# Performance work log

Measured on AMD Instinct MI355X. Metric: run time of the kernel, lower is better.

The kernel has to match this reference:

```python
import jax, jax.numpy as jnp
import numpy as np

N, E, F_IN, EDIM, H = 50000, 1600000, 128, 16, 4
C1, C2, G, NCLS = 32, 8, 64, 10
NEG_SLOPE = 0.2


def setup_inputs() -> dict:
    key = jax.random.key(0)
    ks = jax.random.split(key, 20)
    s = 0.1
    inp = {
        "x": jax.random.normal(ks[0], (N, F_IN), jnp.float32),
        "edge_index": jax.random.randint(ks[1], (2, E), 0, N, dtype=jnp.int32),
        "edge_attr": jax.random.normal(ks[2], (E, EDIM), jnp.float32),
        "batch": jnp.sort(jax.random.randint(ks[3], (N,), 0, G, dtype=jnp.int32)),
        # layer 1 params (PyG GATConv: shared lin for src/dst, no lin bias)
        "W1": jax.random.normal(ks[4], (F_IN, H * C1), jnp.float32) * s,
        "as1": jax.random.normal(ks[5], (H, C1), jnp.float32) * s,
        "ad1": jax.random.normal(ks[6], (H, C1), jnp.float32) * s,
        "We1": jax.random.normal(ks[7], (EDIM, H * C1), jnp.float32) * s,
        "ae1": jax.random.normal(ks[8], (H, C1), jnp.float32) * s,
        "b1": jnp.zeros((H * C1,), jnp.float32),
        # layer 2 params
        "W2": jax.random.normal(ks[9], (H * C1, H * C2), jnp.float32) * s,
        "as2": jax.random.normal(ks[10], (H, C2), jnp.float32) * s,
        "ad2": jax.random.normal(ks[11], (H, C2), jnp.float32) * s,
        "We2": jax.random.normal(ks[12], (EDIM, H * C2), jnp.float32) * s,
        "ae2": jax.random.normal(ks[13], (H, C2), jnp.float32) * s,
        "b2": jnp.zeros((H * C2,), jnp.float32),
        # final linear
        "Wfc": jax.random.normal(ks[14], (H * C2, NCLS), jnp.float32) * s,
        "bfc": jnp.zeros((NCLS,), jnp.float32),
    }
    return inp


def _add_self_loops(src, dst, edge_attr):
    # PyG default: add_self_loops=True, fill_value='mean' (mean of incoming edge attrs)
    deg = jax.ops.segment_sum(jnp.ones((E,), jnp.float32), dst, num_segments=N)
    loop_attr = jax.ops.segment_sum(edge_attr, dst, num_segments=N) / jnp.maximum(deg, 1.0)[:, None]
    loop = jnp.arange(N, dtype=src.dtype)
    return (jnp.concatenate([src, loop]), jnp.concatenate([dst, loop]),
            jnp.concatenate([edge_attr, loop_attr], axis=0))


def _gat_layer(x, src, dst, ea, W, a_src, a_dst, We, a_e, b, heads, ch):
    n = x.shape[0]
    h = (x @ W).reshape(n, heads, ch)                 # [N,H,C]
    he = (ea @ We).reshape(-1, heads, ch)             # [Ef,H,C]
    al_src = jnp.einsum('nhc,hc->nh', h, a_src)       # [N,H]
    al_dst = jnp.einsum('nhc,hc->nh', h, a_dst)
    al_e = jnp.einsum('ehc,hc->eh', he, a_e)          # [Ef,H]
    alpha = al_src[src] + al_dst[dst] + al_e
    alpha = jax.nn.leaky_relu(alpha, NEG_SLOPE)
    # edge softmax grouped by destination node
    amax = jax.ops.segment_max(alpha, dst, num_segments=n)
    alpha = jnp.exp(alpha - amax[dst])
    denom = jax.ops.segment_sum(alpha, dst, num_segments=n)
    alpha = alpha / (denom[dst] + 1e-16)
    out = jax.ops.segment_sum(h[src] * alpha[..., None], dst, num_segments=n)  # [N,H,C]
    return out.reshape(n, heads * ch) + b


def reference(x, edge_index, edge_attr, batch, W1, as1, ad1, We1, ae1, b1,
              W2, as2, ad2, We2, ae2, b2, Wfc, bfc):
    src, dst = edge_index[0], edge_index[1]
    src, dst, ea = _add_self_loops(src, dst, edge_attr)
    h = jax.nn.relu(_gat_layer(x, src, dst, ea, W1, as1, ad1, We1, ae1, b1, H, C1))
    h = jax.nn.relu(_gat_layer(h, src, dst, ea, W2, as2, ad2, We2, ae2, b2, H, C2))
    # global mean pool over graphs
    cnt = jax.ops.segment_sum(jnp.ones((N,), jnp.float32), batch, num_segments=G)
    pooled = jax.ops.segment_sum(h, batch, num_segments=G) / jnp.maximum(cnt, 1.0)[:, None]
    return pooled @ Wfc + bfc
```

## Files before the change

kernel.cpp:

```cpp
#include <hip/hip_runtime.h>
#include <hip/hip_fp16.h>
#include <math.h>

typedef float4 f4;
#define NEG_SLOPE 0.2f
#define NBMAX 1024
#define BIN_CHUNK 8192

union h4pack { float2 f; __half2 h[2]; };

__global__ void k_prep(const float* __restrict__ We1, const float* __restrict__ ae1,
                       const float* __restrict__ We2, const float* __restrict__ ae2,
                       float* __restrict__ M) {
    int t = threadIdx.x;
    if (t >= 128) return;
    int sel = t >> 6, i = t & 63, d = i >> 2, h = i & 3;
    const float* W  = sel ? We2 : We1;
    const float* ae = sel ? ae2 : ae1;
    int C = sel ? 8 : 32, ncol = sel ? 32 : 128;
    float s = 0.f;
    for (int c = 0; c < C; ++c) s += W[d * ncol + h * C + c] * ae[h * C + c];
    M[sel * 64 + d * 4 + h] = s;
}

__global__ __launch_bounds__(256) void k_bhist(const int* __restrict__ ei,
                                               int* __restrict__ bcnt, int E, int NB) {
    __shared__ int hist[NBMAX];
    for (int i = threadIdx.x; i < NB; i += 256) hist[i] = 0;
    __syncthreads();
    int stride = gridDim.x * 256;
    for (int e = blockIdx.x * 256 + threadIdx.x; e < E; e += stride)
        atomicAdd(&hist[ei[E + e] >> 6], 1);
    __syncthreads();
    for (int i = threadIdx.x; i < NB; i += 256) {
        int h = hist[i];
        if (h) atomicAdd(&bcnt[i], h);
    }
}

__global__ void k_bscan(const int* __restrict__ bcnt, int* __restrict__ bprefix,
                        int* __restrict__ bcursor, int NB) {
    __shared__ int ts[NBMAX];
    int t = threadIdx.x;
    ts[t] = (t < NB) ? bcnt[t] : 0;
    __syncthreads();
    for (int off = 1; off < 1024; off <<= 1) {
        int v = (t >= off) ? ts[t - off] : 0;
        __syncthreads();
        ts[t] += v;
        __syncthreads();
    }
    int excl = (t == 0) ? 0 : ts[t - 1];
    if (t <= NB) {
        bprefix[t] = excl;
        if (t < NB) bcursor[t] = excl;
    }
}

__global__ void k_ale_lin(const float* __restrict__ ea, const float* __restrict__ Mbuf,
                          __half* __restrict__ ale1_e, __half* __restrict__ ale2_e, int E) {
    __shared__ float Ms[128];
    if (threadIdx.x < 128) Ms[threadIdx.x] = Mbuf[threadIdx.x];
    __syncthreads();
    int e = blockIdx.x * 256 + threadIdx.x;
    if (e >= E) return;
    const f4* row = (const f4*)(ea + (size_t)e * 16);
    f4 r0 = row[0], r1 = row[1], r2 = row[2], r3 = row[3];
    float a[16] = { r0.x, r0.y, r0.z, r0.w, r1.x, r1.y, r1.z, r1.w,
                    r2.x, r2.y, r2.z, r2.w, r3.x, r3.y, r3.z, r3.w };
    float s10 = 0.f, s11 = 0.f, s12 = 0.f, s13 = 0.f;
    float s20 = 0.f, s21 = 0.f, s22 = 0.f, s23 = 0.f;
#pragma unroll
    for (int dd = 0; dd < 16; ++dd) {
        float av = a[dd];
        s10 += av * Ms[dd * 4 + 0]; s11 += av * Ms[dd * 4 + 1];
        s12 += av * Ms[dd * 4 + 2]; s13 += av * Ms[dd * 4 + 3];
        s20 += av * Ms[64 + dd * 4 + 0]; s21 += av * Ms[64 + dd * 4 + 1];
        s22 += av * Ms[64 + dd * 4 + 2]; s23 += av * Ms[64 + dd * 4 + 3];
    }
    h4pack p1, p2;
    p1.h[0] = __floats2half2_rn(s10, s11); p1.h[1] = __floats2half2_rn(s12, s13);
    p2.h[0] = __floats2half2_rn(s20, s21); p2.h[1] = __floats2half2_rn(s22, s23);
    ((float2*)ale1_e)[e] = p1.f;
    ((float2*)ale2_e)[e] = p2.f;
}

__global__ __launch_bounds__(256) void k_bin(const int* __restrict__ ei,
                                             int* __restrict__ bcursor,
                                             int2* __restrict__ binned, int E, int NB) {
    __shared__ int hist[NBMAX], base[NBMAX], cur[NBMAX];
    for (int i = threadIdx.x; i < NB; i += 256) { hist[i] = 0; cur[i] = 0; }
    __syncthreads();
    int e0 = blockIdx.x * BIN_CHUNK;
    int e1 = min(e0 + BIN_CHUNK, E);
    for (int e = e0 + threadIdx.x; e < e1; e += 256)
        atomicAdd(&hist[ei[E + e] >> 6], 1);
    __syncthreads();
    for (int i = threadIdx.x; i < NB; i += 256) {
        int h = hist[i];
        if (h) base[i] = atomicAdd(&bcursor[i], h);
    }
    __syncthreads();
    for (int e = e0 + threadIdx.x; e < e1; e += 256) {
        int sr = ei[e], d = ei[E + e];
        int b = d >> 6;
        int loc = base[b] + atomicAdd(&cur[b], 1);
        binned[loc] = make_int2(sr, ((d & 63) << 26) | e);
    }
}

__global__ __launch_bounds__(256) void k_csr(const int2* __restrict__ binned,
                                             const int* __restrict__ bprefix,
                                             int* __restrict__ offsets,
                                             int* __restrict__ csr_src,
                                             int* __restrict__ csr_eid,
                                             int N, int E, int NB) {
    __shared__ int nhist[64], noff[65];
    int b = blockIdx.x;
    if (threadIdx.x < 64) nhist[threadIdx.x] = 0;
    __syncthreads();
    int lo = bprefix[b], hi = bprefix[b + 1];
    for (int s = lo + threadIdx.x; s < hi; s += 256)
        atomicAdd(&nhist[(binned[s].y >> 26) & 63], 1);
    __syncthreads();
    if (threadIdx.x == 0) {
        int run = 0;
        for (int i = 0; i < 64; ++i) { noff[i] = run; run += nhist[i]; }
        noff[64] = run;
    }
    __syncthreads();
    int nlo = b << 6;
    int nbn = min(64, N - nlo);
    if (threadIdx.x < nbn) offsets[nlo + threadIdx.x] = lo + noff[threadIdx.x];
    if (b == NB - 1 && threadIdx.x == 0) offsets[N] = E;
    if (threadIdx.x < 64) nhist[threadIdx.x] = 0;
    __syncthreads();
    for (int s = lo + threadIdx.x; s < hi; s += 256) {
        int2 r = binned[s];
        int dl = (r.y >> 26) & 63;
        int slot = lo + noff[dl] + atomicAdd(&nhist[dl], 1);
        csr_src[slot] = r.x;
        csr_eid[slot] = r.y & 0x03FFFFFF;
    }
}

template<int NOUT, int ROWS>
__global__ __launch_bounds__(256) void k_gemm(const float* __restrict__ X,
                                              const float* __restrict__ W,
                                              __half* __restrict__ Hout, int N) {
    __shared__ __align__(16) float xs[ROWS][128];
    int row0 = blockIdx.x * ROWS;
    int tid = threadIdx.x;
    constexpr int NF4 = ROWS * 32;
    const f4* x4 = (const f4*)X;
    for (int i = tid; i < NF4; i += 256) {
        int r = i >> 5, k4 = i & 31;
        f4 v;
        if (row0 + r < N) v = x4[(size_t)(row0 + r) * 32 + k4];
        else { v.x = v.y = v.z = v.w = 0.f; }
        ((f4*)&xs[r][0])[k4] = v;
    }
    __syncthreads();
    constexpr int GRP = 256 / NOUT;
    constexpr int PR  = ROWS / GRP;
    int col = tid % NOUT, rg = tid / NOUT;
    float acc[PR];
#pragma unroll
    for (int r = 0; r < PR; ++r) acc[r] = 0.f;
    for (int k = 0; k < 128; ++k) {
        float w = W[k * NOUT + col];
#pragma unroll
        for (int r = 0; r < PR; ++r) acc[r] += xs[rg + r * GRP][k] * w;
    }
#pragma unroll
    for (int r = 0; r < PR; ++r) {
        int row = row0 + rg + r * GRP;
        if (row < N) Hout[(size_t)row * NOUT + col] = __float2half(acc[r]);
    }
}

template<int C>
__global__ void k_al(const __half* __restrict__ Hm, const float* __restrict__ as_,
                     const float* __restrict__ ad_, float* __restrict__ als,
                     float* __restrict__ ald, int N) {
    int idx = blockIdx.x * 256 + threadIdx.x;
    int n = idx >> 2, h = idx & 3;
    if (n >= N) return;
    constexpr int CH = C / 4;
    const __half2* h2p = (const __half2*)(Hm + (size_t)n * C + h * CH);
    float a = 0.f, b = 0.f;
#pragma unroll
    for (int c = 0; c < CH / 2; ++c) {
        float2 v = __half22float2(h2p[c]);
        a += v.x * as_[h * CH + 2 * c] + v.y * as_[h * CH + 2 * c + 1];
        b += v.x * ad_[h * CH + 2 * c] + v.y * ad_[h * CH + 2 * c + 1];
    }
    als[n * 4 + h] = a;
    ald[n * 4 + h] = b;
}

__global__ __launch_bounds__(256) void k_alpha_node(const __half* __restrict__ ale_e,
                                                    __half* __restrict__ alpha_csr,
                                                    const int* __restrict__ csr_src,
                                                    const int* __restrict__ csr_eid,
                                                    const float* __restrict__ als,
                                                    const float* __restrict__ ald,
                                                    const int* __restrict__ offsets,
                                                    float* __restrict__ rden,
                                                    float* __restrict__ selfa, int N) {
    int n = (blockIdx.x * 256 + threadIdx.x) >> 6;
    int lane = threadIdx.x & 63;
    if (n >= N) return;
    int j = lane >> 2, h = lane & 3;
    int s0 = offsets[n], s1 = offsets[n + 1];
    float aldn = ald[n * 4 + h];
    float den = 0.f, asum = 0.f;
    for (int base = s0; base < s1; base += 16) {
        int s = base + j;
        if (s < s1) {
            int src = csr_src[s];
            int eid = csr_eid[s];
            float ale = __half2float(ale_e[(size_t)eid * 4 + h]);
            float v = als[src * 4 + h] + aldn + ale;
            v = (v > 0.f) ? v : NEG_SLOPE * v;
            float e = __expf(v);
            alpha_csr[s * 4 + h] = __float2half(e);
            den += e; asum += ale;
        }
    }
    den  += __shfl_xor(den, 4);  den  += __shfl_xor(den, 8);
    den  += __shfl_xor(den, 16); den  += __shfl_xor(den, 32);
    asum += __shfl_xor(asum, 4);  asum += __shfl_xor(asum, 8);
    asum += __shfl_xor(asum, 16); asum += __shfl_xor(asum, 32);
    if (j == 0) {
        float rdeg = 1.f / fmaxf((float)(s1 - s0), 1.f);
        float v = als[n * 4 + h] + aldn + asum * rdeg;
        v = (v > 0.f) ? v : NEG_SLOPE * v;
        float es = __expf(v);
        selfa[n * 4 + h] = es;
        rden[n * 4 + h] = 1.f / (den + es + 1e-16f);
    }
}

__global__ __launch_bounds__(256) void k_aggf128(const __half* __restrict__ h16,
                                                 const __half* __restrict__ alpha16,
                                                 const float* __restrict__ rden,
                                                 const float* __restrict__ selfa,
                                                 const int* __restrict__ offsets,
                                                 const int* __restrict__ csr_src,
                                                 const float* __restrict__ bias,
                                                 float* __restrict__ Out, int N) {
    int n = (blockIdx.x * 256 + threadIdx.x) >> 6;
    int lane = threadIdx.x & 63;
    if (n >= N) return;
    int hd = lane >> 4;
    int s0 = offsets[n], s1 = offsets[n + 1];
    const __half2* H2 = (const __half2*)h16;
    float acc0 = 0.f, acc1 = 0.f;
    int e1 = s1 - 1;
    for (int s = s0; s < s1; s += 8) {
        int srck[8]; float ak[8]; __half2 hvk[8];
#pragma unroll
        for (int k = 0; k < 8; ++k) {
            int sk = min(s + k, e1);
            srck[k] = csr_src[sk];
            ak[k] = (s + k <= e1) ? __half2float(alpha16[(size_t)sk * 4 + hd]) : 0.f;
        }
#pragma unroll
        for (int k = 0; k < 8; ++k) hvk[k] = H2[(size_t)srck[k] * 64 + lane];
#pragma unroll
        for (int k = 0; k < 8; ++k) {
            float2 f = __half22float2(hvk[k]);
            acc0 = fmaf(ak[k], f.x, acc0);
            acc1 = fmaf(ak[k], f.y, acc1);
        }
    }
    float sa = selfa[n * 4 + hd];
    float2 hn = __half22float2(H2[(size_t)n * 64 + lane]);
    acc0 = fmaf(sa, hn.x, acc0);
    acc1 = fmaf(sa, hn.y, acc1);
    float rd = rden[n * 4 + hd];
    float2 bv = ((const float2*)bias)[lane];
    float2 o;
    o.x = fmaxf(fmaf(acc0, rd, bv.x), 0.f);
    o.y = fmaxf(fmaf(acc1, rd, bv.y), 0.f);
    ((float2*)Out)[(size_t)n * 64 + lane] = o;
}

__global__ __launch_bounds__(256) void k_aggf32(const __half* __restrict__ h16,
                                                const __half* __restrict__ alpha16,
                                                const float* __restrict__ rden,
                                                const float* __restrict__ selfa,
                                                const int* __restrict__ offsets,
                                                const int* __restrict__ csr_src,
                                                const float* __restrict__ bias,
                                                float* __restrict__ Out, int N) {
    int n = (blockIdx.x * 256 + threadIdx.x) >> 6;
    int lane = threadIdx.x & 63;
    if (n >= N) return;
    int j = lane >> 4;
    int p = lane & 15;
    int hd = p >> 2;
    int s0 = offsets[n], s1 = offsets[n + 1];
    const __half2* H2 = (const __half2*)h16;
    float acc0 = 0.f, acc1 = 0.f;
    int e1 = s1 - 1;
    for (int s = s0 + j; s < s1; s += 8) {
        int sA = s;
        int sB = min(s + 4, e1);
        int srcA = csr_src[sA], srcB = csr_src[sB];
        float aA = __half2float(alpha16[(size_t)sA * 4 + hd]);
        float aB = (s + 4 <= e1) ? __half2float(alpha16[(size_t)sB * 4 + hd]) : 0.f;
        __half2 hA = H2[(size_t)srcA * 16 + p];
        __half2 hB = H2[(size_t)srcB * 16 + p];
        float2 fA = __half22float2(hA), fB = __half22float2(hB);
        acc0 = fmaf(aA, fA.x, acc0); acc1 = fmaf(aA, fA.y, acc1);
        acc0 = fmaf(aB, fB.x, acc0); acc1 = fmaf(aB, fB.y, acc1);
    }
    acc0 += __shfl_xor(acc0, 16); acc0 += __shfl_xor(acc0, 32);
    acc1 += __shfl_xor(acc1, 16); acc1 += __shfl_xor(acc1, 32);
    if (j == 0) {
        float sa = selfa[n * 4 + hd];
        float2 hn = __half22float2(H2[(size_t)n * 16 + p]);
        acc0 = fmaf(sa, hn.x, acc0);
        acc1 = fmaf(sa, hn.y, acc1);
        float rd = rden[n * 4 + hd];
        float2 bv = ((const float2*)bias)[p];
        float2 o;
        o.x = fmaxf(fmaf(acc0, rd, bv.x), 0.f);
        o.y = fmaxf(fmaf(acc1, rd, bv.y), 0.f);
        ((float2*)Out)[(size_t)n * 16 + p] = o;
    }
}

__global__ void k_gbound(const int* __restrict__ batch, int* __restrict__ gstart, int N, int G) {
    int g = threadIdx.x;
    if (g > G) return;
    int lo = 0, hi = N;
    while (lo < hi) {
        int mid = (lo + hi) >> 1;
        if (batch[mid] < g) lo = mid + 1; else hi = mid;
    }
    gstart[g] = lo;
}

__global__ __launch_bounds__(256) void k_pool_grp(const float* __restrict__ out2,
                                                  const int* __restrict__ gstart,
                                                  float* __restrict__ pooled, int G) {
    __shared__ float red[8][32];
    int g = blockIdx.x;
    int t = threadIdx.x, c = t & 31, r = t >> 5;
    int s0 = gstart[g], s1 = gstart[g + 1];
    float acc = 0.f;
    for (int n = s0 + r; n < s1; n += 8) acc += out2[(size_t)n * 32 + c];
    red[r][c] = acc;
    __syncthreads();
    if (r == 0) {
        float s = red[0][c];
#pragma unroll
        for (int i = 1; i < 8; ++i) s += red[i][c];
        pooled[g * 32 + c] = s;
    }
}

__global__ void k_final(const float* __restrict__ pooled, const int* __restrict__ gstart,
                        const float* __restrict__ Wfc, const float* __restrict__ bfc,
                        float* __restrict__ out) {
    int t = threadIdx.x;
    if (t >= 640) return;
    int g = t / 10, cls = t % 10;
    float rc = 1.f / fmaxf((float)(gstart[g + 1] - gstart[g]), 1.f);
    float acc = bfc[cls];
    for (int c = 0; c < 32; ++c) acc += pooled[g * 32 + c] * rc * Wfc[c * 10 + cls];
    out[g * 10 + cls] = acc;
}

extern "C" void kernel_launch(void* const* d_in, const int* in_sizes, int n_in,
                              void* d_out, int out_size, void* d_ws, size_t ws_size,
                              hipStream_t stream) {
    const float* x    = (const float*)d_in[0];
    const int*   ei   = (const int*)  d_in[1];
    const float* ea   = (const float*)d_in[2];
    const int*   batch= (const int*)  d_in[3];
    const float* W1   = (const float*)d_in[4];
    const float* as1  = (const float*)d_in[5];
    const float* ad1  = (const float*)d_in[6];
    const float* We1  = (const float*)d_in[7];
    const float* ae1  = (const float*)d_in[8];
    const float* b1   = (const float*)d_in[9];
    const float* W2   = (const float*)d_in[10];
    const float* as2  = (const float*)d_in[11];
    const float* ad2  = (const float*)d_in[12];
    const float* We2  = (const float*)d_in[13];
    const float* ae2  = (const float*)d_in[14];
    const float* b2   = (const float*)d_in[15];
    const float* Wfc  = (const float*)d_in[16];
    const float* bfc  = (const float*)d_in[17];
    float* out = (float*)d_out;

    const int N  = in_sizes[3];
    const int E  = in_sizes[1] / 2;
    const int G  = 64;
    const int NB = (N + 63) >> 6;

    char* w = (char*)d_ws;
    size_t off = 0;
    auto alloc = [&](size_t bytes) -> void* {
        void* p = w + off;
        off = (off + bytes + 255) & ~(size_t)255;
        return p;
    };
    int*    bcnt       = (int*)   alloc((size_t)NBMAX * 4);
    int*    bprefix    = (int*)   alloc((size_t)(NBMAX + 1) * 4);
    int*    bcursor    = (int*)   alloc((size_t)NBMAX * 4);
    int*    offsets    = (int*)   alloc((size_t)(N + 1) * 4);
    int2*   binned     = (int2*)  alloc((size_t)E * 8);
    __half* ale1_e     = (__half*)alloc((size_t)E * 4 * 2);
    __half* ale2_e     = (__half*)alloc((size_t)E * 4 * 2);
    int*    csr_src    = (int*)   alloc((size_t)E * 4);
    int*    csr_eid    = (int*)   alloc((size_t)E * 4);
    float*  Mbuf       = (float*) alloc(128 * 4);
    __half* h16        = (__half*)alloc((size_t)N * 128 * 2);
    float*  out1       = (float*) alloc((size_t)N * 128 * 4);
    float*  als        = (float*) alloc((size_t)N * 4 * 4);
    float*  ald        = (float*) alloc((size_t)N * 4 * 4);
    float*  rden       = (float*) alloc((size_t)N * 4 * 4);
    float*  selfa      = (float*) alloc((size_t)N * 4 * 4);
    int*    gstart     = (int*)   alloc((G + 1) * 4);
    float*  pooled     = (float*) alloc(G * 32 * 4);
    __half* alpha_csr  = (__half*)binned;
    float*  out2 = out1;

    const int eb  = (E + 255) / 256;
    const int nb4 = (N + 3) / 4;

    hipMemsetAsync(bcnt, 0, (size_t)NBMAX * 4, stream);

    k_prep<<<1, 128, 0, stream>>>(We1, ae1, We2, ae2, Mbuf);
    k_bhist<<<128, 256, 0, stream>>>(ei, bcnt, E, NB);
    k_bscan<<<1, 1024, 0, stream>>>(bcnt, bprefix, bcursor, NB);
    k_ale_lin<<<eb, 256, 0, stream>>>(ea, Mbuf, ale1_e, ale2_e, E);
    k_bin<<<(E + BIN_CHUNK - 1) / BIN_CHUNK, 256, 0, stream>>>(ei, bcursor, binned, E, NB);
    k_csr<<<NB, 256, 0, stream>>>(binned, bprefix, offsets, csr_src, csr_eid, N, E, NB);
    k_gbound<<<1, 128, 0, stream>>>(batch, gstart, N, G);

    k_gemm<128, 16><<<(N + 15) / 16, 256, 0, stream>>>(x, W1, h16, N);
    k_al<128><<<(N * 4 + 255) / 256, 256, 0, stream>>>(h16, as1, ad1, als, ald, N);
    k_alpha_node<<<nb4, 256, 0, stream>>>(ale1_e, alpha_csr, csr_src, csr_eid, als, ald, offsets, rden, selfa, N);
    k_aggf128<<<nb4, 256, 0, stream>>>(h16, alpha_csr, rden, selfa, offsets, csr_src, b1, out1, N);

    k_gemm<32, 64><<<(N + 63) / 64, 256, 0, stream>>>(out1, W2, h16, N);
    k_al<32><<<(N * 4 + 255) / 256, 256, 0, stream>>>(h16, as2, ad2, als, ald, N);
    k_alpha_node<<<nb4, 256, 0, stream>>>(ale2_e, alpha_csr, csr_src, csr_eid, als, ald, offsets, rden, selfa, N);
    k_aggf32<<<nb4, 256, 0, stream>>>(h16, alpha_csr, rden, selfa, offsets, csr_src, b2, out2, N);

    k_pool_grp<<<G, 256, 0, stream>>>(out2, gstart, pooled, G);
    k_final<<<1, 640, 0, stream>>>(pooled, gstart, Wfc, bfc, out);
}
```

Baseline: 393.1 us.

## Fuse edge-softmax attention computation into the aggregation kernels

Removes the separate per-node alpha kernel and computes unnormalised attention weights, the denominator and the self-loop weight inside each aggregation kernel, normalising at the end. This drops the fp16 alpha_csr write and read plus the rden/selfa buffers, and saves two launches per forward. In exchange, in the 128-wide kernel every lane redundantly gathers csr_eid, ale and als and computes the exp for its head (16x duplication across channel lanes), which adds scattered loads and ALU work.

```diff
diff --git a/kernel.cpp b/kernel.cpp
--- a/kernel.cpp
+++ b/kernel.cpp
@@ -199,87 +199,58 @@
     ald[n * 4 + h] = b;
 }
 
-__global__ __launch_bounds__(256) void k_alpha_node(const __half* __restrict__ ale_e,
-                                                    __half* __restrict__ alpha_csr,
-                                                    const int* __restrict__ csr_src,
-                                                    const int* __restrict__ csr_eid,
-                                                    const float* __restrict__ als,
-                                                    const float* __restrict__ ald,
-                                                    const int* __restrict__ offsets,
-                                                    float* __restrict__ rden,
-                                                    float* __restrict__ selfa, int N) {
-    int n = (blockIdx.x * 256 + threadIdx.x) >> 6;
-    int lane = threadIdx.x & 63;
-    if (n >= N) return;
-    int j = lane >> 2, h = lane & 3;
-    int s0 = offsets[n], s1 = offsets[n + 1];
-    float aldn = ald[n * 4 + h];
-    float den = 0.f, asum = 0.f;
-    for (int base = s0; base < s1; base += 16) {
-        int s = base + j;
-        if (s < s1) {
-            int src = csr_src[s];
-            int eid = csr_eid[s];
-            float ale = __half2float(ale_e[(size_t)eid * 4 + h]);
-            float v = als[src * 4 + h] + aldn + ale;
-            v = (v > 0.f) ? v : NEG_SLOPE * v;
-            float e = __expf(v);
-            alpha_csr[s * 4 + h] = __float2half(e);
-            den += e; asum += ale;
-        }
-    }
-    den  += __shfl_xor(den, 4);  den  += __shfl_xor(den, 8);
-    den  += __shfl_xor(den, 16); den  += __shfl_xor(den, 32);
-    asum += __shfl_xor(asum, 4);  asum += __shfl_xor(asum, 8);
-    asum += __shfl_xor(asum, 16); asum += __shfl_xor(asum, 32);
-    if (j == 0) {
-        float rdeg = 1.f / fmaxf((float)(s1 - s0), 1.f);
-        float v = als[n * 4 + h] + aldn + asum * rdeg;
-        v = (v > 0.f) ? v : NEG_SLOPE * v;
-        float es = __expf(v);
-        selfa[n * 4 + h] = es;
-        rden[n * 4 + h] = 1.f / (den + es + 1e-16f);
-    }
-}
-
-__global__ __launch_bounds__(256) void k_aggf128(const __half* __restrict__ h16,
-                                                 const __half* __restrict__ alpha16,
-                                                 const float* __restrict__ rden,
-                                                 const float* __restrict__ selfa,
-                                                 const int* __restrict__ offsets,
-                                                 const int* __restrict__ csr_src,
-                                                 const float* __restrict__ bias,
-                                                 float* __restrict__ Out, int N) {
+__global__ __launch_bounds__(256) void k_aggfu128(const __half* __restrict__ h16,
+                                                  const __half* __restrict__ ale_e,
+                                                  const float* __restrict__ als,
+                                                  const float* __restrict__ ald,
+                                                  const int* __restrict__ offsets,
+                                                  const int* __restrict__ csr_src,
+                                                  const int* __restrict__ csr_eid,
+                                                  const float* __restrict__ bias,
+                                                  float* __restrict__ Out, int N) {
     int n = (blockIdx.x * 256 + threadIdx.x) >> 6;
     int lane = threadIdx.x & 63;
     if (n >= N) return;
     int hd = lane >> 4;
     int s0 = offsets[n], s1 = offsets[n + 1];
+    float aldn = ald[n * 4 + hd];
     const __half2* H2 = (const __half2*)h16;
-    float acc0 = 0.f, acc1 = 0.f;
+    float acc0 = 0.f, acc1 = 0.f, den = 0.f, asum = 0.f;
     int e1 = s1 - 1;
     for (int s = s0; s < s1; s += 8) {
-        int srck[8]; float ak[8]; __half2 hvk[8];
+        int srck[8]; float ek[8]; __half2 hvk[8];
 #pragma unroll
         for (int k = 0; k < 8; ++k) {
             int sk = min(s + k, e1);
             srck[k] = csr_src[sk];
-            ak[k] = (s + k <= e1) ? __half2float(alpha16[(size_t)sk * 4 + hd]) : 0.f;
+            int eid = csr_eid[sk];
+            bool valid = (s + k <= e1);
+            float ale = __half2float(ale_e[(size_t)eid * 4 + hd]);
+            float v = als[srck[k] * 4 + hd] + aldn + ale;
+            v = (v > 0.f) ? v : NEG_SLOPE * v;
+            float e = valid ? __expf(v) : 0.f;
+            ek[k] = e;
+            den += e;
+            asum += valid ? ale : 0.f;
         }
 #pragma unroll
         for (int k = 0; k < 8; ++k) hvk[k] = H2[(size_t)srck[k] * 64 + lane];
 #pragma unroll
         for (int k = 0; k < 8; ++k) {
             float2 f = __half22float2(hvk[k]);
-            acc0 = fmaf(ak[k], f.x, acc0);
-            acc1 = fmaf(ak[k], f.y, acc1);
+            acc0 = fmaf(ek[k], f.x, acc0);
+            acc1 = fmaf(ek[k], f.y, acc1);
         }
     }
-    float sa = selfa[n * 4 + hd];
+    float rdeg = 1.f / fmaxf((float)(s1 - s0), 1.f);
+    float vs = als[n * 4 + hd] + aldn + asum * rdeg;
+    vs = (vs > 0.f) ? vs : NEG_SLOPE * vs;
+    float es = __expf(vs);
     float2 hn = __half22float2(H2[(size_t)n * 64 + lane]);
-    acc0 = fmaf(sa, hn.x, acc0);
-    acc1 = fmaf(sa, hn.y, acc1);
-    float rd = rden[n * 4 + hd];
+    acc0 = fmaf(es, hn.x, acc0);
+    acc1 = fmaf(es, hn.y, acc1);
+    den += es;
+    float rd = 1.f / (den + 1e-16f);
     float2 bv = ((const float2*)bias)[lane];
     float2 o;
     o.x = fmaxf(fmaf(acc0, rd, bv.x), 0.f);
@@ -287,14 +258,15 @@
     ((float2*)Out)[(size_t)n * 64 + lane] = o;
 }
 
-__global__ __launch_bounds__(256) void k_aggf32(const __half* __restrict__ h16,
-                                                const __half* __restrict__ alpha16,
-                                                const float* __restrict__ rden,
-                                                const float* __restrict__ selfa,
-                                                const int* __restrict__ offsets,
-                                                const int* __restrict__ csr_src,
-                                                const float* __restrict__ bias,
-                                                float* __restrict__ Out, int N) {
+__global__ __launch_bounds__(256) void k_aggfu32(const __half* __restrict__ h16,
+                                                 const __half* __restrict__ ale_e,
+                                                 const float* __restrict__ als,
+                                                 const float* __restrict__ ald,
+                                                 const int* __restrict__ offsets,
+                                                 const int* __restrict__ csr_src,
+                                                 const int* __restrict__ csr_eid,
+                                                 const float* __restrict__ bias,
+                                                 float* __restrict__ Out, int N) {
     int n = (blockIdx.x * 256 + threadIdx.x) >> 6;
     int lane = threadIdx.x & 63;
     if (n >= N) return;
@@ -302,29 +274,46 @@
     int p = lane & 15;
     int hd = p >> 2;
     int s0 = offsets[n], s1 = offsets[n + 1];
+    float aldn = ald[n * 4 + hd];
     const __half2* H2 = (const __half2*)h16;
-    float acc0 = 0.f, acc1 = 0.f;
+    float acc0 = 0.f, acc1 = 0.f, den = 0.f, asum = 0.f;
     int e1 = s1 - 1;
     for (int s = s0 + j; s < s1; s += 8) {
         int sA = s;
         int sB = min(s + 4, e1);
+        bool vB = (s + 4 <= e1);
         int srcA = csr_src[sA], srcB = csr_src[sB];
-        float aA = __half2float(alpha16[(size_t)sA * 4 + hd]);
-        float aB = (s + 4 <= e1) ? __half2float(alpha16[(size_t)sB * 4 + hd]) : 0.f;
+        int eidA = csr_eid[sA], eidB = csr_eid[sB];
+        float aleA = __half2float(ale_e[(size_t)eidA * 4 + hd]);
+        float aleB = __half2float(ale_e[(size_t)eidB * 4 + hd]);
+        float vA = als[srcA * 4 + hd] + aldn + aleA;
+        float vBv = als[srcB * 4 + hd] + aldn + aleB;
+        vA = (vA > 0.f) ? vA : NEG_SLOPE * vA;
+        vBv = (vBv > 0.f) ? vBv : NEG_SLOPE * vBv;
+        float eA = __expf(vA);
+        float eB = vB ? __expf(vBv) : 0.f;
+        den += eA + eB;
+        asum += aleA + (vB ? aleB : 0.f);
         __half2 hA = H2[(size_t)srcA * 16 + p];
         __half2 hB = H2[(size_t)srcB * 16 + p];
         float2 fA = __half22float2(hA), fB = __half22float2(hB);
-        acc0 = fmaf(aA, fA.x, acc0); acc1 = fmaf(aA, fA.y, acc1);
-        acc0 = fmaf(aB, fB.x, acc0); acc1 = fmaf(aB, fB.y, acc1);
+        acc0 = fmaf(eA, fA.x, acc0); acc1 = fmaf(eA, fA.y, acc1);
+        acc0 = fmaf(eB, fB.x, acc0); acc1 = fmaf(eB, fB.y, acc1);
     }
     acc0 += __shfl_xor(acc0, 16); acc0 += __shfl_xor(acc0, 32);
     acc1 += __shfl_xor(acc1, 16); acc1 += __shfl_xor(acc1, 32);
+    den  += __shfl_xor(den, 16);  den  += __shfl_xor(den, 32);
+    asum += __shfl_xor(asum, 16); asum += __shfl_xor(asum, 32);
     if (j == 0) {
-        float sa = selfa[n * 4 + hd];
+        float rdeg = 1.f / fmaxf((float)(s1 - s0), 1.f);
+        float vs = als[n * 4 + hd] + aldn + asum * rdeg;
+        vs = (vs > 0.f) ? vs : NEG_SLOPE * vs;
+        float es = __expf(vs);
         float2 hn = __half22float2(H2[(size_t)n * 16 + p]);
-        acc0 = fmaf(sa, hn.x, acc0);
-        acc1 = fmaf(sa, hn.y, acc1);
-        float rd = rden[n * 4 + hd];
+        acc0 = fmaf(es, hn.x, acc0);
+        acc1 = fmaf(es, hn.y, acc1);
+        den += es;
+        float rd = 1.f / (den + 1e-16f);
         float2 bv = ((const float2*)bias)[p];
         float2 o;
         o.x = fmaxf(fmaf(acc0, rd, bv.x), 0.f);
@@ -424,11 +413,8 @@
     float*  out1       = (float*) alloc((size_t)N * 128 * 4);
     float*  als        = (float*) alloc((size_t)N * 4 * 4);
     float*  ald        = (float*) alloc((size_t)N * 4 * 4);
-    float*  rden       = (float*) alloc((size_t)N * 4 * 4);
-    float*  selfa      = (float*) alloc((size_t)N * 4 * 4);
     int*    gstart     = (int*)   alloc((G + 1) * 4);
     float*  pooled     = (float*) alloc(G * 32 * 4);
-    __half* alpha_csr  = (__half*)binned;
     float*  out2 = out1;
 
     const int eb  = (E + 255) / 256;
@@ -446,13 +432,11 @@
 
     k_gemm<128, 16><<<(N + 15) / 16, 256, 0, stream>>>(x, W1, h16, N);
     k_al<128><<<(N * 4 + 255) / 256, 256, 0, stream>>>(h16, as1, ad1, als, ald, N);
-    k_alpha_node<<<nb4, 256, 0, stream>>>(ale1_e, alpha_csr, csr_src, csr_eid, als, ald, offsets, rden, selfa, N);
-    k_aggf128<<<nb4, 256, 0, stream>>>(h16, alpha_csr, rden, selfa, offsets, csr_src, b1, out1, N);
+    k_aggfu128<<<nb4, 256, 0, stream>>>(h16, ale1_e, als, ald, offsets, csr_src, csr_eid, b1, out1, N);
 
     k_gemm<32, 64><<<(N + 63) / 64, 256, 0, stream>>>(out1, W2, h16, N);
     k_al<32><<<(N * 4 + 255) / 256, 256, 0, stream>>>(h16, as2, ad2, als, ald, N);
-    k_alpha_node<<<nb4, 256, 0, stream>>>(ale2_e, alpha_csr, csr_src, csr_eid, als, ald, offsets, rden, selfa, N);
-    k_aggf32<<<nb4, 256, 0, stream>>>(h16, alpha_csr, rden, selfa, offsets, csr_src, b2, out2, N);
+    k_aggfu32<<<nb4, 256, 0, stream>>>(h16, ale2_e, als, ald, offsets, csr_src, csr_eid, b2, out2, N);
 
     k_pool_grp<<<G, 256, 0, stream>>>(out2, gstart, pooled, G);
     k_final<<<1, 640, 0, stream>>>(pooled, gstart, Wfc, bfc, out);
```

New measurement: 435.5 us. +10.8%, slower.
